# Kernel tuning notes

Hardware: AMD Instinct MI355X
Metric: run time of the kernel (lower is better)

## Reference

```python
import jax, jax.numpy as jnp
import numpy as np

B, N, D, P, K = 4, 2048, 512, 16, 4
EPS_BW = 1e-8
EPS_LN = 1e-5


def setup_inputs() -> dict:
    key = jax.random.key(0)
    ks = jax.random.split(key, 8)
    charge = jax.random.normal(ks[0], (B, N, D), dtype=jnp.float32)
    position = jax.random.normal(ks[1], (B, N, P), dtype=jnp.float32)
    mass = jax.random.uniform(ks[2], (B, N, 1), dtype=jnp.float32)
    # parameters
    log_bandwidth = jnp.zeros((K,), dtype=jnp.float32)
    W_charge = jax.random.normal(ks[3], (D * K, D), dtype=jnp.float32) / np.sqrt(D)   # torch Linear weight (out,in)
    W_combine = jax.random.normal(ks[4], (D, D * K), dtype=jnp.float32) / np.sqrt(D * K)
    gamma = jnp.ones((D,), dtype=jnp.float32)
    beta = jnp.zeros((D,), dtype=jnp.float32)
    return {"charge": charge, "position": position, "mass": mass,
            "log_bandwidth": log_bandwidth, "W_charge": W_charge,
            "W_combine": W_combine, "gamma": gamma, "beta": beta}


def reference(charge, position, mass, log_bandwidth, W_charge, W_combine, gamma, beta):
    # pairwise squared distances: (B, N, N)
    diff = position[:, :, None, :] - position[:, None, :, :]
    dist_sq = jnp.sum(diff * diff, axis=-1)
    # multi-bandwidth Gaussian kernels: (B, N, N, K)
    bandwidths = jnp.exp(log_bandwidth)
    kernels = jnp.exp(-dist_sq[..., None] / (2.0 * bandwidths + EPS_BW))
    # mass weighting: mass (B,N,1) -> (B,1,N,1), broadcast over query axis and kernels
    weighted_kernels = kernels * mass[:, None, :, :]
    # project charges: (B, N, K, D)
    projected = (charge @ W_charge.T).reshape(B, N, K, D)
    # aggregate over neighbours j: field[b,i,k,d] = sum_j wk[b,i,j,k] * proj[b,j,k,d]
    field = jnp.einsum('bijk,bjkd->bikd', weighted_kernels, projected)
    field = field.reshape(B, N, K * D) @ W_combine.T  # (B, N, D)
    # LayerNorm
    mean = jnp.mean(field, axis=-1, keepdims=True)
    var = jnp.var(field, axis=-1, keepdims=True)
    normed = (field - mean) * jax.lax.rsqrt(var + EPS_LN)
    return normed * gamma + beta
```

## Files before the change

kernel.cpp:

```cpp
#include <hip/hip_runtime.h>


typedef __bf16 bf16x8 __attribute__((ext_vector_type(8)));
typedef float f32x4 __attribute__((ext_vector_type(4)));

__device__ __forceinline__ unsigned short f2bf(float f) {
    unsigned u = __float_as_uint(f);
    unsigned r = (u + 0x7fffu + ((u >> 16) & 1u)) >> 16;
    return (unsigned short)r;
}
__device__ __forceinline__ float bf2f(unsigned short h) {
    return __uint_as_float(((unsigned)h) << 16);
}
__device__ __forceinline__ void g2l16(const unsigned short* g, unsigned short* l) {
    __builtin_amdgcn_global_load_lds(
        (const __attribute__((address_space(1))) unsigned int*)g,
        (__attribute__((address_space(3))) unsigned int*)l, 16, 0, 0);
}

__global__ __launch_bounds__(256) void k0_pos(const float* __restrict__ pos,
                                              unsigned short* __restrict__ posA,
                                              unsigned short* __restrict__ posB1,
                                              unsigned short* __restrict__ posB2,
                                              float* __restrict__ rsq)
{
    const int row = blockIdx.x * 256 + threadIdx.x;
    const float* src = &pos[(size_t)row * 16];
    float p[16];
#pragma unroll
    for (int cc = 0; cc < 4; cc++) {
        float4 v = *reinterpret_cast<const float4*>(&src[cc * 4]);
        p[cc * 4 + 0] = v.x; p[cc * 4 + 1] = v.y; p[cc * 4 + 2] = v.z; p[cc * 4 + 3] = v.w;
    }
    float r = 0.f;
    unsigned short h[16], lo[16], z[8] = {0, 0, 0, 0, 0, 0, 0, 0};
#pragma unroll
    for (int d = 0; d < 16; d++) {
        r = __builtin_fmaf(p[d], p[d], r);
        h[d] = f2bf(p[d]);
        lo[d] = f2bf(p[d] - bf2f(h[d]));
    }
    rsq[row] = r;
    size_t o = (size_t)row * 32;
    *reinterpret_cast<int4*>(&posA[o + 0])   = *reinterpret_cast<int4*>(&h[0]);
    *reinterpret_cast<int4*>(&posA[o + 8])   = *reinterpret_cast<int4*>(&h[8]);
    *reinterpret_cast<int4*>(&posA[o + 16])  = *reinterpret_cast<int4*>(&lo[0]);
    *reinterpret_cast<int4*>(&posA[o + 24])  = *reinterpret_cast<int4*>(&lo[8]);
    *reinterpret_cast<int4*>(&posB1[o + 0])  = *reinterpret_cast<int4*>(&h[0]);
    *reinterpret_cast<int4*>(&posB1[o + 8])  = *reinterpret_cast<int4*>(&h[8]);
    *reinterpret_cast<int4*>(&posB1[o + 16]) = *reinterpret_cast<int4*>(&h[0]);
    *reinterpret_cast<int4*>(&posB1[o + 24]) = *reinterpret_cast<int4*>(&h[8]);
    *reinterpret_cast<int4*>(&posB2[o + 0])  = *reinterpret_cast<int4*>(&lo[0]);
    *reinterpret_cast<int4*>(&posB2[o + 8])  = *reinterpret_cast<int4*>(&lo[8]);
    *reinterpret_cast<int4*>(&posB2[o + 16]) = *reinterpret_cast<int4*>(&z[0]);
    *reinterpret_cast<int4*>(&posB2[o + 24]) = *reinterpret_cast<int4*>(&z[0]);
}

__global__ __launch_bounds__(256) void k0_cvt(const float* __restrict__ src,
                                              unsigned short* __restrict__ dst)
{
    size_t i = (size_t)blockIdx.x * 256 + threadIdx.x;
    float4 v = reinterpret_cast<const float4*>(src)[i];
    unsigned short o[4] = {f2bf(v.x), f2bf(v.y), f2bf(v.z), f2bf(v.w)};
    reinterpret_cast<uint2*>(dst)[i] = *reinterpret_cast<uint2*>(&o[0]);
}

__global__ __launch_bounds__(256, 2) void k1_proj(const unsigned short* __restrict__ wc16,
                                                  const unsigned short* __restrict__ ch16,
                                                  const float* __restrict__ mass,
                                                  unsigned short* __restrict__ projm_t)
{
    __shared__ alignas(16) unsigned short As[128 * 32];
    __shared__ alignas(16) unsigned short Bs[128 * 32];
    const int tid = threadIdx.x, lane = tid & 63, wid = tid >> 6;
    const int q = lane >> 4, l15 = lane & 15;
    const int m0 = blockIdx.y * 128, n0 = blockIdx.x * 128;
    const int wm = (wid & 1) * 64, wn = (wid >> 1) * 64;

    f32x4 acc[4][4];
#pragma unroll
    for (int i = 0; i < 4; i++)
#pragma unroll
        for (int j = 0; j < 4; j++) acc[i][j] = (f32x4){0.f, 0.f, 0.f, 0.f};

    for (int k0 = 0; k0 < 512; k0 += 32) {
        __syncthreads();
#pragma unroll
        for (int q4 = 0; q4 < 4; q4++) {
            int chunk = q4 * 256 + tid;
            int w = chunk & 511, row = w >> 2, c4 = w & 3;
            if (chunk < 512)
                g2l16(&wc16[(size_t)(m0 + row) * 512 + k0 + c4 * 8], &As[w * 8]);
            else
                g2l16(&ch16[(size_t)(n0 + row) * 512 + k0 + c4 * 8], &Bs[w * 8]);
        }
        __syncthreads();
        bf16x8 af[4], bfr[4];
#pragma unroll
        for (int it = 0; it < 4; it++)
            af[it] = *reinterpret_cast<const bf16x8*>(&As[(wm + it * 16 + l15) * 32 + q * 8]);
#pragma unroll
        for (int ct = 0; ct < 4; ct++)
            bfr[ct] = *reinterpret_cast<const bf16x8*>(&Bs[(wn + ct * 16 + l15) * 32 + q * 8]);
#pragma unroll
        for (int it = 0; it < 4; it++)
#pragma unroll
            for (int ct = 0; ct < 4; ct++)
                acc[it][ct] = __builtin_amdgcn_mfma_f32_16x16x32_bf16(af[it], bfr[ct], acc[it][ct], 0, 0, 0);
    }
#pragma unroll
    for (int ct = 0; ct < 4; ct++) {
        int n = n0 + wn + ct * 16 + l15;
        float mf = mass[n];
#pragma unroll
        for (int it = 0; it < 4; it++) {
            int mrow = m0 + wm + it * 16 + q * 4;
#pragma unroll
            for (int r = 0; r < 4; r++)
                projm_t[(size_t)(mrow + r) * 8192 + n] = f2bf(acc[it][ct][r] * mf);
        }
    }
}

__global__ __launch_bounds__(256, 2) void k2_field(const unsigned short* __restrict__ posA,
                                                   const unsigned short* __restrict__ posB1,
                                                   const unsigned short* __restrict__ posB2,
                                                   const float* __restrict__ rsq,
                                                   const float* __restrict__ logbw,
                                                   const unsigned short* __restrict__ projm_t,
                                                   unsigned short* __restrict__ field)
{
    __shared__ alignas(16) unsigned short Bs[2][256 * 32];
    __shared__ alignas(16) unsigned short pB1[2][32 * 32];
    __shared__ alignas(16) unsigned short pB2[2][32 * 32];
    __shared__ alignas(16) unsigned short Wl[2][128 * 40];

    const int tid = threadIdx.x, lane = tid & 63, wid = tid >> 6;
    const int q = lane >> 4, l15 = lane & 15;
    const int L = blockIdx.x;
    const int xcd = L & 7, idx = L >> 3;
    const int i_t = idx & 15, cb = xcd * 4 + (idx >> 4);
    const int c0 = (cb & 7) * 256, b = cb >> 3;
    const int i0 = i_t * 128;
    const int kb = c0 >> 9;
    const float bw = __expf(logbw[kb]);
    const float s2 = -1.4426950408889634f / (2.0f * bw + 1e-8f);
    const float c2 = -2.0f * s2;

    bf16x8 afG[2];
    float riv[2][4];
#pragma unroll
    for (int t = 0; t < 2; t++) {
        afG[t] = *reinterpret_cast<const bf16x8*>(
            &posA[(size_t)(b * 2048 + i0 + wid * 32 + t * 16 + l15) * 32 + q * 8]);
#pragma unroll
        for (int r = 0; r < 4; r++)
            riv[t][r] = rsq[b * 2048 + i0 + wid * 32 + t * 16 + q * 4 + r];
    }

    const int wo_i = (wid >> 1) * 64, wo_c = (wid & 1) * 128;

    f32x4 acc[4][8];
#pragma unroll
    for (int i = 0; i < 4; i++)
#pragma unroll
        for (int j = 0; j < 8; j++) acc[i][j] = (f32x4){0.f, 0.f, 0.f, 0.f};

    for (int j0 = 0; j0 < 2048; j0 += 64) {
        float rjv[2][2];
#pragma unroll
        for (int s = 0; s < 2; s++)
#pragma unroll
            for (int jt2 = 0; jt2 < 2; jt2++)
                rjv[s][jt2] = rsq[b * 2048 + j0 + s * 32 + jt2 * 16 + l15];

        __syncthreads();
        {
            const size_t gb = (size_t)c0 * 8192 + b * 2048 + j0;
#pragma unroll
            for (int q8 = 0; q8 < 8; q8++) {
                int chunk = q8 * 256 + tid;
                int s = chunk >> 10, w1 = chunk & 1023;
                g2l16(&projm_t[gb + (size_t)(w1 >> 2) * 8192 + s * 32 + (w1 & 3) * 8],
                      &Bs[s][w1 * 8]);
            }
        }
        {
            const size_t gp = (size_t)(b * 2048 + j0) * 32;
#pragma unroll
            for (int q2 = 0; q2 < 2; q2++) {
                int chunk = q2 * 256 + tid;
                int w = chunk & 255, s = w >> 7, w2 = w & 127;
                if (chunk < 256)
                    g2l16(&posB1[gp + s * 1024 + w2 * 8], &pB1[s][w2 * 8]);
                else
                    g2l16(&posB2[gp + s * 1024 + w2 * 8], &pB2[s][w2 * 8]);
            }
        }
        __syncthreads();
#pragma unroll
        for (int s = 0; s < 2; s++) {
#pragma unroll
            for (int jt2 = 0; jt2 < 2; jt2++) {
                bf16x8 b2 = *reinterpret_cast<const bf16x8*>(&pB2[s][(jt2 * 16 + l15) * 32 + q * 8]);
                bf16x8 b1 = *reinterpret_cast<const bf16x8*>(&pB1[s][(jt2 * 16 + l15) * 32 + q * 8]);
#pragma unroll
                for (int t = 0; t < 2; t++) {
                    f32x4 g = (f32x4){0.f, 0.f, 0.f, 0.f};
                    g = __builtin_amdgcn_mfma_f32_16x16x32_bf16(afG[t], b2, g, 0, 0, 0);
                    g = __builtin_amdgcn_mfma_f32_16x16x32_bf16(afG[t], b1, g, 0, 0, 0);
                    float rj = rjv[s][jt2];
#pragma unroll
                    for (int r = 0; r < 4; r++) {
                        float x = __builtin_fmaf(g[r], c2, (riv[t][r] + rj) * s2);
                        Wl[s][(wid * 32 + t * 16 + q * 4 + r) * 40 + (jt2 * 16 + l15)] =
                            f2bf(__builtin_amdgcn_exp2f(x));
                    }
                }
            }
        }
        __syncthreads();
#pragma unroll
        for (int s = 0; s < 2; s++) {
            bf16x8 af[4], bfr[8];
#pragma unroll
            for (int it = 0; it < 4; it++)
                af[it] = *reinterpret_cast<const bf16x8*>(&Wl[s][(wo_i + it * 16 + l15) * 40 + q * 8]);
#pragma unroll
            for (int ct = 0; ct < 8; ct++)
                bfr[ct] = *reinterpret_cast<const bf16x8*>(&Bs[s][(wo_c + ct * 16 + l15) * 32 + q * 8]);
#pragma unroll
            for (int it = 0; it < 4; it++)
#pragma unroll
                for (int ct = 0; ct < 8; ct++)
                    acc[it][ct] = __builtin_amdgcn_mfma_f32_16x16x32_bf16(af[it], bfr[ct], acc[it][ct], 0, 0, 0);
        }
    }
#pragma unroll
    for (int it = 0; it < 4; it++) {
#pragma unroll
        for (int ct = 0; ct < 8; ct++) {
            int gi = b * 2048 + i0 + wo_i + it * 16 + q * 4;
            int gc = c0 + wo_c + ct * 16 + l15;
#pragma unroll
            for (int r = 0; r < 4; r++)
                field[(size_t)(gi + r) * 2048 + gc] = f2bf(acc[it][ct][r]);
        }
    }
}

__global__ __launch_bounds__(256, 2) void k3_combine(const unsigned short* __restrict__ field,
                                                     const unsigned short* __restrict__ wcb16,
                                                     float* __restrict__ out)
{
    __shared__ alignas(16) unsigned short As[64 * 32];
    __shared__ alignas(16) unsigned short Bs[128 * 32];
    const int tid = threadIdx.x, lane = tid & 63, wid = tid >> 6;
    const int q = lane >> 4, l15 = lane & 15;
    const int m0 = blockIdx.y * 64, n0 = blockIdx.x * 128;
    const int wn = wid * 32;

    f32x4 acc[4][2];
#pragma unroll
    for (int i = 0; i < 4; i++)
#pragma unroll
        for (int j = 0; j < 2; j++) acc[i][j] = (f32x4){0.f, 0.f, 0.f, 0.f};

    for (int k0 = 0; k0 < 2048; k0 += 32) {
        __syncthreads();
#pragma unroll
        for (int q3 = 0; q3 < 3; q3++) {
            int chunk = q3 * 256 + tid;
            if (chunk < 256) {
                int row = chunk >> 2, c4 = chunk & 3;
                g2l16(&field[(size_t)(m0 + row) * 2048 + k0 + c4 * 8], &As[chunk * 8]);
            } else {
                int w = chunk - 256, row = w >> 2, c4 = w & 3;
                g2l16(&wcb16[(size_t)(n0 + row) * 2048 + k0 + c4 * 8], &Bs[w * 8]);
            }
        }
        __syncthreads();
        bf16x8 af[4], bfr[2];
#pragma unroll
        for (int it = 0; it < 4; it++)
            af[it] = *reinterpret_cast<const bf16x8*>(&As[(it * 16 + l15) * 32 + q * 8]);
#pragma unroll
        for (int ct = 0; ct < 2; ct++)
            bfr[ct] = *reinterpret_cast<const bf16x8*>(&Bs[(wn + ct * 16 + l15) * 32 + q * 8]);
#pragma unroll
        for (int it = 0; it < 4; it++)
#pragma unroll
            for (int ct = 0; ct < 2; ct++)
                acc[it][ct] = __builtin_amdgcn_mfma_f32_16x16x32_bf16(af[it], bfr[ct], acc[it][ct], 0, 0, 0);
    }
#pragma unroll
    for (int it = 0; it < 4; it++) {
#pragma unroll
        for (int ct = 0; ct < 2; ct++) {
            int m = m0 + it * 16 + q * 4;
            int n = n0 + wn + ct * 16 + l15;
#pragma unroll
            for (int r = 0; r < 4; r++)
                out[(size_t)(m + r) * 512 + n] = acc[it][ct][r];
        }
    }
}

__global__ __launch_bounds__(256) void k4_ln(float* __restrict__ out,
                                             const float* __restrict__ gamma,
                                             const float* __restrict__ beta)
{
    __shared__ float red[8];
    const int row = blockIdx.x, tid = threadIdx.x;
    float2 x = *reinterpret_cast<const float2*>(&out[(size_t)row * 512 + tid * 2]);
    float s = x.x + x.y;
    float ss = x.x * x.x + x.y * x.y;
#pragma unroll
    for (int off = 32; off > 0; off >>= 1) {
        s += __shfl_down(s, off);
        ss += __shfl_down(ss, off);
    }
    int wid = tid >> 6;
    if ((tid & 63) == 0) { red[wid * 2] = s; red[wid * 2 + 1] = ss; }
    __syncthreads();
    s = red[0] + red[2] + red[4] + red[6];
    ss = red[1] + red[3] + red[5] + red[7];
    float mean = s * (1.f / 512.f);
    float var = ss * (1.f / 512.f) - mean * mean;
    float inv = rsqrtf(var + 1e-5f);
    float g0 = gamma[tid * 2], g1 = gamma[tid * 2 + 1];
    float b0 = beta[tid * 2], b1 = beta[tid * 2 + 1];
    float2 o;
    o.x = (x.x - mean) * inv * g0 + b0;
    o.y = (x.y - mean) * inv * g1 + b1;
    *reinterpret_cast<float2*>(&out[(size_t)row * 512 + tid * 2]) = o;
}

extern "C" void kernel_launch(void* const* d_in, const int* in_sizes, int n_in,
                              void* d_out, int out_size, void* d_ws, size_t ws_size,
                              hipStream_t stream)
{
    const float* charge   = (const float*)d_in[0];
    const float* position = (const float*)d_in[1];
    const float* mass     = (const float*)d_in[2];
    const float* logbw    = (const float*)d_in[3];
    const float* Wc       = (const float*)d_in[4];
    const float* Wcb      = (const float*)d_in[5];
    const float* gamma    = (const float*)d_in[6];
    const float* beta     = (const float*)d_in[7];

    unsigned short* projm_t = (unsigned short*)d_ws;
    unsigned short* field   = projm_t + (size_t)2048 * 8192;
    unsigned short* wcb16   = projm_t;
    unsigned short* ch16    = field;
    unsigned short* wc16    = field + (size_t)8192 * 512;
    unsigned short* posA  = (unsigned short*)d_out;
    unsigned short* posB1 = posA + (size_t)8192 * 32;
    unsigned short* posB2 = posB1 + (size_t)8192 * 32;
    float* rsq = (float*)(posB2 + (size_t)8192 * 32);
    float* out = (float*)d_out;

    k0_pos<<<32, 256, 0, stream>>>(position, posA, posB1, posB2, rsq);
    k0_cvt<<<4096, 256, 0, stream>>>(charge, ch16);
    k0_cvt<<<1024, 256, 0, stream>>>(Wc, wc16);
    k1_proj<<<dim3(64, 16), 256, 0, stream>>>(wc16, ch16, mass, projm_t);
    k2_field<<<512, 256, 0, stream>>>(posA, posB1, posB2, rsq, logbw, projm_t, field);
    k0_cvt<<<1024, 256, 0, stream>>>(Wcb, wcb16);
    k3_combine<<<dim3(4, 128), 256, 0, stream>>>(field, wcb16, out);
    k4_ln<<<8192, 256, 0, stream>>>(out, gamma, beta);
}
```

Baseline: 263.2 us.

## XOR-swizzle LDS tiles and restructure field kernel to compute weights from global

```diff
diff --git a/kernel.cpp b/kernel.cpp
--- a/kernel.cpp
+++ b/kernel.cpp
@@ -74,6 +74,7 @@
     __shared__ alignas(16) unsigned short Bs[128 * 32];
     const int tid = threadIdx.x, lane = tid & 63, wid = tid >> 6;
     const int q = lane >> 4, l15 = lane & 15;
+    const int sw = (l15 >> 2) & 3;
     const int m0 = blockIdx.y * 128, n0 = blockIdx.x * 128;
     const int wm = (wid & 1) * 64, wn = (wid >> 1) * 64;
 
@@ -88,20 +89,21 @@
 #pragma unroll
         for (int q4 = 0; q4 < 4; q4++) {
             int chunk = q4 * 256 + tid;
-            int w = chunk & 511, row = w >> 2, c4 = w & 3;
+            int w = chunk & 511, row = w >> 2;
+            int gc4 = (w & 3) ^ ((w >> 4) & 3);
             if (chunk < 512)
-                g2l16(&wc16[(size_t)(m0 + row) * 512 + k0 + c4 * 8], &As[w * 8]);
+                g2l16(&wc16[(size_t)(m0 + row) * 512 + k0 + gc4 * 8], &As[w * 8]);
             else
-                g2l16(&ch16[(size_t)(n0 + row) * 512 + k0 + c4 * 8], &Bs[w * 8]);
+                g2l16(&ch16[(size_t)(n0 + row) * 512 + k0 + gc4 * 8], &Bs[w * 8]);
         }
         __syncthreads();
         bf16x8 af[4], bfr[4];
 #pragma unroll
         for (int it = 0; it < 4; it++)
-            af[it] = *reinterpret_cast<const bf16x8*>(&As[(wm + it * 16 + l15) * 32 + q * 8]);
+            af[it] = *reinterpret_cast<const bf16x8*>(&As[(wm + it * 16 + l15) * 32 + (q ^ sw) * 8]);
 #pragma unroll
         for (int ct = 0; ct < 4; ct++)
-            bfr[ct] = *reinterpret_cast<const bf16x8*>(&Bs[(wn + ct * 16 + l15) * 32 + q * 8]);
+            bfr[ct] = *reinterpret_cast<const bf16x8*>(&Bs[(wn + ct * 16 + l15) * 32 + (q ^ sw) * 8]);
 #pragma unroll
         for (int it = 0; it < 4; it++)
 #pragma unroll
@@ -131,12 +133,11 @@
                                                    unsigned short* __restrict__ field)
 {
     __shared__ alignas(16) unsigned short Bs[2][256 * 32];
-    __shared__ alignas(16) unsigned short pB1[2][32 * 32];
-    __shared__ alignas(16) unsigned short pB2[2][32 * 32];
     __shared__ alignas(16) unsigned short Wl[2][128 * 40];
 
     const int tid = threadIdx.x, lane = tid & 63, wid = tid >> 6;
     const int q = lane >> 4, l15 = lane & 15;
+    const int sw = (l15 >> 2) & 3;
     const int L = blockIdx.x;
     const int xcd = L & 7, idx = L >> 3;
     const int i_t = idx & 15, cb = xcd * 4 + (idx >> 4);
@@ -146,16 +147,17 @@
     const float bw = __expf(logbw[kb]);
     const float s2 = -1.4426950408889634f / (2.0f * bw + 1e-8f);
     const float c2 = -2.0f * s2;
+    const int bN = b * 2048;
 
     bf16x8 afG[2];
-    float riv[2][4];
+    float riS2[2][4];
 #pragma unroll
     for (int t = 0; t < 2; t++) {
         afG[t] = *reinterpret_cast<const bf16x8*>(
-            &posA[(size_t)(b * 2048 + i0 + wid * 32 + t * 16 + l15) * 32 + q * 8]);
+            &posA[(size_t)(bN + i0 + wid * 32 + t * 16 + l15) * 32 + q * 8]);
 #pragma unroll
         for (int r = 0; r < 4; r++)
-            riv[t][r] = rsq[b * 2048 + i0 + wid * 32 + t * 16 + q * 4 + r];
+            riS2[t][r] = rsq[bN + i0 + wid * 32 + t * 16 + q * 4 + r] * s2;
     }
 
     const int wo_i = (wid >> 1) * 64, wo_c = (wid & 1) * 128;
@@ -167,60 +169,51 @@
         for (int j = 0; j < 8; j++) acc[i][j] = (f32x4){0.f, 0.f, 0.f, 0.f};
 
     for (int j0 = 0; j0 < 2048; j0 += 64) {
-        float rjv[2][2];
-#pragma unroll
-        for (int s = 0; s < 2; s++)
-#pragma unroll
-            for (int jt2 = 0; jt2 < 2; jt2++)
-                rjv[s][jt2] = rsq[b * 2048 + j0 + s * 32 + jt2 * 16 + l15];
-
-        __syncthreads();
-        {
-            const size_t gb = (size_t)c0 * 8192 + b * 2048 + j0;
-#pragma unroll
-            for (int q8 = 0; q8 < 8; q8++) {
-                int chunk = q8 * 256 + tid;
-                int s = chunk >> 10, w1 = chunk & 1023;
-                g2l16(&projm_t[gb + (size_t)(w1 >> 2) * 8192 + s * 32 + (w1 & 3) * 8],
-                      &Bs[s][w1 * 8]);
-            }
-        }
-        {
-            const size_t gp = (size_t)(b * 2048 + j0) * 32;
-#pragma unroll
-            for (int q2 = 0; q2 < 2; q2++) {
-                int chunk = q2 * 256 + tid;
-                int w = chunk & 255, s = w >> 7, w2 = w & 127;
-                if (chunk < 256)
-                    g2l16(&posB1[gp + s * 1024 + w2 * 8], &pB1[s][w2 * 8]);
-                else
-                    g2l16(&posB2[gp + s * 1024 + w2 * 8], &pB2[s][w2 * 8]);
-            }
-        }
-        __syncthreads();
+        unsigned short wv[2][2][2][4];
 #pragma unroll
         for (int s = 0; s < 2; s++) {
 #pragma unroll
             for (int jt2 = 0; jt2 < 2; jt2++) {
-                bf16x8 b2 = *reinterpret_cast<const bf16x8*>(&pB2[s][(jt2 * 16 + l15) * 32 + q * 8]);
-                bf16x8 b1 = *reinterpret_cast<const bf16x8*>(&pB1[s][(jt2 * 16 + l15) * 32 + q * 8]);
+                int j = bN + j0 + s * 32 + jt2 * 16 + l15;
+                bf16x8 b1 = *reinterpret_cast<const bf16x8*>(&posB1[(size_t)j * 32 + q * 8]);
+                bf16x8 b2 = *reinterpret_cast<const bf16x8*>(&posB2[(size_t)j * 32 + q * 8]);
+                float rj2 = rsq[j] * s2;
 #pragma unroll
                 for (int t = 0; t < 2; t++) {
                     f32x4 g = (f32x4){0.f, 0.f, 0.f, 0.f};
                     g = __builtin_amdgcn_mfma_f32_16x16x32_bf16(afG[t], b2, g, 0, 0, 0);
                     g = __builtin_amdgcn_mfma_f32_16x16x32_bf16(afG[t], b1, g, 0, 0, 0);
-                    float rj = rjv[s][jt2];
 #pragma unroll
                     for (int r = 0; r < 4; r++) {
-                        float x = __builtin_fmaf(g[r], c2, (riv[t][r] + rj) * s2);
-                        Wl[s][(wid * 32 + t * 16 + q * 4 + r) * 40 + (jt2 * 16 + l15)] =
-                            f2bf(__builtin_amdgcn_exp2f(x));
+                        float x = __builtin_fmaf(g[r], c2, riS2[t][r] + rj2);
+                        wv[s][jt2][t][r] = f2bf(__builtin_amdgcn_exp2f(x));
                     }
                 }
             }
         }
         __syncthreads();
 #pragma unroll
+        for (int s = 0; s < 2; s++)
+#pragma unroll
+            for (int jt2 = 0; jt2 < 2; jt2++)
+#pragma unroll
+                for (int t = 0; t < 2; t++)
+#pragma unroll
+                    for (int r = 0; r < 4; r++)
+                        Wl[s][(wid * 32 + t * 16 + q * 4 + r) * 40 + jt2 * 16 + l15] =
+                            wv[s][jt2][t][r];
+        {
+            const size_t gb = (size_t)c0 * 8192 + bN + j0;
+#pragma unroll
+            for (int q8 = 0; q8 < 8; q8++) {
+                int chunk = q8 * 256 + tid;
+                int s = chunk >> 10, w1 = chunk & 1023;
+                int row = w1 >> 2, gc4 = (w1 & 3) ^ ((w1 >> 4) & 3);
+                g2l16(&projm_t[gb + (size_t)row * 8192 + s * 32 + gc4 * 8], &Bs[s][w1 * 8]);
+            }
+        }
+        __syncthreads();
+#pragma unroll
         for (int s = 0; s < 2; s++) {
             bf16x8 af[4], bfr[8];
 #pragma unroll
@@ -228,7 +221,7 @@
                 af[it] = *reinterpret_cast<const bf16x8*>(&Wl[s][(wo_i + it * 16 + l15) * 40 + q * 8]);
 #pragma unroll
             for (int ct = 0; ct < 8; ct++)
-                bfr[ct] = *reinterpret_cast<const bf16x8*>(&Bs[s][(wo_c + ct * 16 + l15) * 32 + q * 8]);
+                bfr[ct] = *reinterpret_cast<const bf16x8*>(&Bs[s][(wo_c + ct * 16 + l15) * 32 + (q ^ sw) * 8]);
 #pragma unroll
             for (int it = 0; it < 4; it++)
 #pragma unroll
@@ -240,7 +233,7 @@
     for (int it = 0; it < 4; it++) {
 #pragma unroll
         for (int ct = 0; ct < 8; ct++) {
-            int gi = b * 2048 + i0 + wo_i + it * 16 + q * 4;
+            int gi = bN + i0 + wo_i + it * 16 + q * 4;
             int gc = c0 + wo_c + ct * 16 + l15;
 #pragma unroll
             for (int r = 0; r < 4; r++)
@@ -257,6 +250,7 @@
     __shared__ alignas(16) unsigned short Bs[128 * 32];
     const int tid = threadIdx.x, lane = tid & 63, wid = tid >> 6;
     const int q = lane >> 4, l15 = lane & 15;
+    const int sw = (l15 >> 2) & 3;
     const int m0 = blockIdx.y * 64, n0 = blockIdx.x * 128;
     const int wn = wid * 32;
 
@@ -272,21 +266,21 @@
         for (int q3 = 0; q3 < 3; q3++) {
             int chunk = q3 * 256 + tid;
             if (chunk < 256) {
-                int row = chunk >> 2, c4 = chunk & 3;
-                g2l16(&field[(size_t)(m0 + row) * 2048 + k0 + c4 * 8], &As[chunk * 8]);
+                int row = chunk >> 2, gc4 = (chunk & 3) ^ ((chunk >> 4) & 3);
+                g2l16(&field[(size_t)(m0 + row) * 2048 + k0 + gc4 * 8], &As[chunk * 8]);
             } else {
-                int w = chunk - 256, row = w >> 2, c4 = w & 3;
-                g2l16(&wcb16[(size_t)(n0 + row) * 2048 + k0 + c4 * 8], &Bs[w * 8]);
+                int w = chunk - 256, row = w >> 2, gc4 = (w & 3) ^ ((w >> 4) & 3);
+                g2l16(&wcb16[(size_t)(n0 + row) * 2048 + k0 + gc4 * 8], &Bs[w * 8]);
             }
         }
         __syncthreads();
         bf16x8 af[4], bfr[2];
 #pragma unroll
         for (int it = 0; it < 4; it++)
-            af[it] = *reinterpret_cast<const bf16x8*>(&As[(it * 16 + l15) * 32 + q * 8]);
+            af[it] = *reinterpret_cast<const bf16x8*>(&As[(it * 16 + l15) * 32 + (q ^ sw) * 8]);
 #pragma unroll
         for (int ct = 0; ct < 2; ct++)
-            bfr[ct] = *reinterpret_cast<const bf16x8*>(&Bs[(wn + ct * 16 + l15) * 32 + q * 8]);
+            bfr[ct] = *reinterpret_cast<const bf16x8*>(&Bs[(wn + ct * 16 + l15) * 32 + (q ^ sw) * 8]);
 #pragma unroll
         for (int it = 0; it < 4; it++)
 #pragma unroll
```

After: 260.8 us. Within noise of the previous version (-0.9%).
